# Kernel optimization log

Hardware: AMD Instinct MI355X
Metric: run time of the kernel (lower is better)

The kernel has to match this reference:

```python
import jax, jax.numpy as jnp
import numpy as np

# Production-scale 3D conv: B=4, C=64->64, 32^3 volume, 3x3x3 kernel, stride 1, pad 1.
B, CIN, COUT = 4, 64, 64
KSIZE = (3, 3, 3)
STRIDE = (1, 1, 1)
PAD = 1
SPATIAL = (32, 32, 32)


def setup_inputs() -> dict:
    key = jax.random.key(0)
    k1, k2, k3 = jax.random.split(key, 3)
    x = jax.random.normal(k1, (B, CIN) + SPATIAL, dtype=jnp.float32)
    weight = jax.random.normal(k2, (COUT, CIN) + KSIZE, dtype=jnp.float32)
    bias = jax.random.normal(k3, (COUT,), dtype=jnp.float32)
    return {"x": x, "weight": weight, "bias": bias}


def reference(x, weight, bias):
    # The original materializes all sliding-window patches via nested unfold and
    # contracts with einsum('bci...,oci->bo...'). That is exactly a standard
    # cross-correlation (torch-style conv). We express the same math as a direct
    # convolution, avoiding the O(kernel_volume) patch blowup.
    out = jax.lax.conv_general_dilated(
        x,
        weight,
        window_strides=STRIDE,
        padding=[(PAD, PAD)] * 3,
        dimension_numbers=("NCDHW", "OIDHW", "NCDHW"),
    )
    return out + bias.reshape(1, -1, 1, 1, 1)
```

## Files before the change

### kernel.cpp

```cpp
#include <hip/hip_runtime.h>
#include <hip/hip_bf16.h>

#define WS_W_OFF    0
#define WS_ZERO_OFF 221184
#define WS_XT_OFF   262144

typedef __attribute__((ext_vector_type(8))) short s16x8;
typedef __attribute__((ext_vector_type(4))) float f32x4;

#define GLOBAL_AS __attribute__((address_space(1)))
#define LDS_AS    __attribute__((address_space(3)))

__device__ __forceinline__ unsigned short f2bf(float f) {
  unsigned u = __builtin_bit_cast(unsigned, f);
  u = u + 0x7fffu + ((u >> 16) & 1u);
  return (unsigned short)(u >> 16);
}

__global__ void prep_kernel(const float* __restrict__ x,
                            const float* __restrict__ w,
                            unsigned short* __restrict__ wsw,
                            float* __restrict__ zeros,
                            unsigned short* __restrict__ xt) {
  int blk = blockIdx.x;
  int tid = threadIdx.x;
  if (blk < 432) {
    int t = blk * 256 + tid;
    int tap  = t % 27;
    int cin  = (t / 27) & 63;
    int cout = t / (27 * 64);
    int h   = cin >> 5;
    int q   = (cin >> 3) & 3;
    int j   = cin & 7;
    int nf  = cout >> 4;
    int lane = q * 16 + (cout & 15);
    int dst = (((tap * 2 + h) * 4 + nf) * 64 + lane) * 8 + j;
    wsw[dst] = f2bf(w[t]);
    if (t < 64) zeros[t] = 0.0f;
  } else {
    __shared__ __align__(16) unsigned char tile[256 * 144];
    int bi = blk - 432;
    int b  = bi >> 7;
    int s0 = (bi & 127) * 256;
    const float* xb = x + (size_t)b * 64 * 32768 + s0 + tid;
    #pragma unroll
    for (int c0 = 0; c0 < 64; c0 += 8) {
      s16x8 v;
      #pragma unroll
      for (int j = 0; j < 8; ++j)
        v[j] = (short)f2bf(xb[(size_t)(c0 + j) * 32768]);
      *(s16x8*)&tile[tid * 144 + c0 * 2] = v;
    }
    __syncthreads();
    #pragma unroll
    for (int it = 0; it < 8; ++it) {
      int row   = it * 32 + (tid >> 3);
      int col16 = tid & 7;
      s16x8 v = *(const s16x8*)&tile[row * 144 + col16 * 16];
      *(s16x8*)(xt + ((size_t)(b * 32768 + s0 + row) * 64 + col16 * 8)) = v;
    }
  }
}

__global__ __launch_bounds__(256, 2) void conv_kernel(const float* __restrict__ bias,
                                                      float* __restrict__ out,
                                                      const char* __restrict__ ws) {
  __shared__ __align__(16) unsigned char halo[52 * 1024];

  const int tid  = threadIdx.x;
  const int lane = tid & 63;
  const int w    = tid >> 6;
  const int logical = (blockIdx.x & 7) * 64 + (blockIdx.x >> 3);
  const int yt = logical & 7, zt = (logical >> 3) & 15, b = logical >> 7;
  const int z0 = zt * 2, y0 = yt * 4;
  const int zo  = w >> 1;
  const int yo2 = (w & 1) * 2;

  const int r15 = lane & 15;
  const int hi4 = lane >> 4;

  const int sl_sub   = lane >> 2;
  const int sl_chunk = lane & 3;

  auto stage_halo = [&](int h) {
    for (int g = w; g < 52; g += 4) {
      int pos = g * 16 + sl_sub;
      int hz = pos / 204; int rem = pos - hz * 204;
      int hy = rem / 34;  int hx = rem - hy * 34;
      int gz = z0 + hz - 1, gy = y0 + hy - 1, gx = hx - 1;
      bool inb = (pos < 816) & ((unsigned)gz < 32u) &
                 ((unsigned)gy < 32u) & ((unsigned)gx < 32u);
      int s = (gz * 32 + gy) * 32 + gx;
      int src = inb ? (WS_XT_OFF + (b * 32768 + s) * 128 + h * 64 + sl_chunk * 16)
                    : WS_ZERO_OFF;
      __builtin_amdgcn_global_load_lds(
          (const GLOBAL_AS void*)(ws + src),
          (LDS_AS void*)(&halo[g * 1024 + lane * 16]),
          16, 0, 0);
    }
  };

  const char* wsb_lane = ws + WS_W_OFF + lane * 16;

  f32x4 zero4 = {0.f, 0.f, 0.f, 0.f};
  f32x4 acc[4][4];
  #pragma unroll
  for (int mf = 0; mf < 4; ++mf)
    #pragma unroll
    for (int nf = 0; nf < 4; ++nf) acc[mf][nf] = zero4;

  s16x8 Bb[3][4];

  auto issueB = [&](int slot, int h, int tap) {
    const char* bt = wsb_lane + (tap * 2 + h) * 4096;
    asm volatile("global_load_dwordx4 %0, %1, off"             : "=v"(Bb[slot][0]) : "v"(bt));
    asm volatile("global_load_dwordx4 %0, %1, off offset:1024" : "=v"(Bb[slot][1]) : "v"(bt));
    asm volatile("global_load_dwordx4 %0, %1, off offset:2048" : "=v"(Bb[slot][2]) : "v"(bt));
    asm volatile("global_load_dwordx4 %0, %1, off offset:3072" : "=v"(Bb[slot][3]) : "v"(bt));
  };

  auto loadA = [&](s16x8* a, int tap) {
    int kd = tap / 9; int r9 = tap - kd * 9;
    int kh = r9 / 3;  int kw = r9 - kh * 3;
    int base = ((zo + kd) * 6 + (yo2 + kh)) * 34 + kw + r15;
    #pragma unroll
    for (int mf = 0; mf < 4; ++mf) {
      int pos = base + (mf >> 1) * 34 + (mf & 1) * 16;
      a[mf] = *(const s16x8*)&halo[pos * 64 + hi4 * 16];
    }
  };

  auto compute = [&](const s16x8* a, const s16x8* B) {
    #pragma unroll
    for (int mf = 0; mf < 4; ++mf)
      #pragma unroll
      for (int nf = 0; nf < 4; ++nf)
        acc[mf][nf] = __builtin_amdgcn_mfma_f32_16x16x32_bf16(
            a[mf], B[nf], acc[mf][nf], 0, 0, 0);
  };

  auto run27 = [&](int h) {
    #pragma unroll
    for (int tap = 0; tap < 27; ++tap) {
      if (tap < 25) issueB((tap + 2) % 3, h, tap + 2);
      if (tap < 25)        { asm volatile("s_waitcnt vmcnt(8)"); }
      else if (tap == 25)  { asm volatile("s_waitcnt vmcnt(4)"); }
      else                 { asm volatile("s_waitcnt vmcnt(0)"); }
      __builtin_amdgcn_sched_barrier(0x106);
      s16x8 Af[4];
      loadA(Af, tap);
      compute(Af, Bb[tap % 3]);
    }
  };

  stage_halo(0);
  issueB(0, 0, 0); issueB(1, 0, 1);
  __syncthreads();
  run27(0);

  issueB(0, 1, 0); issueB(1, 1, 1);
  __syncthreads();
  stage_halo(1);
  __syncthreads();
  run27(1);

  const int z = z0 + zo;
  #pragma unroll
  for (int nf = 0; nf < 4; ++nf) {
    int cout = nf * 16 + r15;
    float bv = bias[cout];
    #pragma unroll
    for (int mf = 0; mf < 4; ++mf) {
      int y  = y0 + yo2 + (mf >> 1);
      int x0 = (mf & 1) * 16 + 4 * hi4;
      float* orow = out + ((size_t)((b * 64 + cout) * 32 + z) * 32 + y) * 32;
      f32x4 v;
      #pragma unroll
      for (int r = 0; r < 4; ++r) v[r] = acc[mf][nf][r] + bv;
      *(f32x4*)&orow[x0] = v;
    }
  }
}

extern "C" void kernel_launch(void* const* d_in, const int* in_sizes, int n_in,
                              void* d_out, int out_size, void* d_ws, size_t ws_size,
                              hipStream_t stream) {
  const float* x    = (const float*)d_in[0];
  const float* wgt  = (const float*)d_in[1];
  const float* bias = (const float*)d_in[2];
  float* out = (float*)d_out;
  char* ws = (char*)d_ws;

  prep_kernel<<<944, 256, 0, stream>>>(x, wgt,
                                       (unsigned short*)(ws + WS_W_OFF),
                                       (float*)(ws + WS_ZERO_OFF),
                                       (unsigned short*)(ws + WS_XT_OFF));
  conv_kernel<<<512, 256, 0, stream>>>(bias, out, ws);
}
```

Before: 44.96 us.

## Stage weights through LDS with double-buffered register prefetch and barriers

Weight tiles are now copied cooperatively into a two-slot LDS buffer with global_load_lds, one 16-byte chunk per thread, so each block fetches a tap's weights once instead of every wave loading its own copy into registers. A/B fragments are prefetched one tap ahead into double-buffered registers, and MFMA issue is wrapped in setprio. This removes redundant global weight traffic per wave but adds several block-wide barriers per tap and more LDS reads. The rotation writing slot t&1 while slot t&1 is also read looks fragile, so the hazard ordering is questionable.

```diff
diff --git a/kernel.cpp b/kernel.cpp
--- a/kernel.cpp
+++ b/kernel.cpp
@@ -66,6 +66,7 @@
                                                       float* __restrict__ out,
                                                       const char* __restrict__ ws) {
   __shared__ __align__(16) unsigned char halo[52 * 1024];
+  __shared__ __align__(16) unsigned char blds[2][4096];
 
   const int tid  = threadIdx.x;
   const int lane = tid & 63;
@@ -100,7 +101,29 @@
     }
   };
 
-  const char* wsb_lane = ws + WS_W_OFF + lane * 16;
+  auto stage_B = [&](int h, int tap, int buf) {
+    __builtin_amdgcn_global_load_lds(
+        (const GLOBAL_AS void*)(ws + WS_W_OFF + (tap * 2 + h) * 4096 + tid * 16),
+        (LDS_AS void*)(&blds[buf][tid * 16]),
+        16, 0, 0);
+  };
+
+  auto loadBlds = [&](s16x8* dst, int buf) {
+    #pragma unroll
+    for (int nf = 0; nf < 4; ++nf)
+      dst[nf] = *(const s16x8*)&blds[buf][(nf * 64 + lane) * 16];
+  };
+
+  auto loadA = [&](s16x8* a, int tap) {
+    int kd = tap / 9; int r9 = tap - kd * 9;
+    int kh = r9 / 3;  int kw = r9 - kh * 3;
+    int base = ((zo + kd) * 6 + (yo2 + kh)) * 34 + kw + r15;
+    #pragma unroll
+    for (int mf = 0; mf < 4; ++mf) {
+      int pos = base + (mf >> 1) * 34 + (mf & 1) * 16;
+      a[mf] = *(const s16x8*)&halo[pos * 64 + hi4 * 16];
+    }
+  };
 
   f32x4 zero4 = {0.f, 0.f, 0.f, 0.f};
   f32x4 acc[4][4];
@@ -109,26 +132,7 @@
     #pragma unroll
     for (int nf = 0; nf < 4; ++nf) acc[mf][nf] = zero4;
 
-  s16x8 Bb[3][4];
-
-  auto issueB = [&](int slot, int h, int tap) {
-    const char* bt = wsb_lane + (tap * 2 + h) * 4096;
-    asm volatile("global_load_dwordx4 %0, %1, off"             : "=v"(Bb[slot][0]) : "v"(bt));
-    asm volatile("global_load_dwordx4 %0, %1, off offset:1024" : "=v"(Bb[slot][1]) : "v"(bt));
-    asm volatile("global_load_dwordx4 %0, %1, off offset:2048" : "=v"(Bb[slot][2]) : "v"(bt));
-    asm volatile("global_load_dwordx4 %0, %1, off offset:3072" : "=v"(Bb[slot][3]) : "v"(bt));
-  };
-
-  auto loadA = [&](s16x8* a, int tap) {
-    int kd = tap / 9; int r9 = tap - kd * 9;
-    int kh = r9 / 3;  int kw = r9 - kh * 3;
-    int base = ((zo + kd) * 6 + (yo2 + kh)) * 34 + kw + r15;
-    #pragma unroll
-    for (int mf = 0; mf < 4; ++mf) {
-      int pos = base + (mf >> 1) * 34 + (mf & 1) * 16;
-      a[mf] = *(const s16x8*)&halo[pos * 64 + hi4 * 16];
-    }
-  };
+  s16x8 Ar[2][4], Br[2][4];
 
   auto compute = [&](const s16x8* a, const s16x8* B) {
     #pragma unroll
@@ -140,27 +144,39 @@
   };
 
   auto run27 = [&](int h) {
-    #pragma unroll
-    for (int tap = 0; tap < 27; ++tap) {
-      if (tap < 25) issueB((tap + 2) % 3, h, tap + 2);
-      if (tap < 25)        { asm volatile("s_waitcnt vmcnt(8)"); }
-      else if (tap == 25)  { asm volatile("s_waitcnt vmcnt(4)"); }
-      else                 { asm volatile("s_waitcnt vmcnt(0)"); }
-      __builtin_amdgcn_sched_barrier(0x106);
-      s16x8 Af[4];
-      loadA(Af, tap);
-      compute(Af, Bb[tap % 3]);
+    loadBlds(Br[0], 0); loadA(Ar[0], 0);
+    asm volatile("s_waitcnt lgkmcnt(0)");
+    __builtin_amdgcn_s_barrier();
+    #pragma unroll
+    for (int t = 0; t < 27; ++t) {
+      const int cur = t & 1, nxt = cur ^ 1;
+      if (t + 2 <= 26) {
+        stage_B(h, t + 2, t & 1);
+        asm volatile("s_waitcnt vmcnt(1)");
+      } else if (t + 1 <= 26) {
+        asm volatile("s_waitcnt vmcnt(0)");
+      }
+      if (t + 1 <= 26) {
+        loadBlds(Br[nxt], (t + 1) & 1);
+        loadA(Ar[nxt], t + 1);
+      }
+      __builtin_amdgcn_s_barrier();
+      asm volatile("s_waitcnt lgkmcnt(0)");
+      __builtin_amdgcn_sched_barrier(0);
+      __builtin_amdgcn_s_setprio(1);
+      compute(Ar[cur], Br[cur]);
+      __builtin_amdgcn_s_setprio(0);
+      __builtin_amdgcn_s_barrier();
     }
   };
 
   stage_halo(0);
-  issueB(0, 0, 0); issueB(1, 0, 1);
+  stage_B(0, 0, 0); stage_B(0, 1, 1);
   __syncthreads();
   run27(0);
 
-  issueB(0, 1, 0); issueB(1, 1, 1);
-  __syncthreads();
   stage_halo(1);
+  stage_B(1, 0, 0); stage_B(1, 1, 1);
   __syncthreads();
   run27(1);
 
```

After: 52.86 us. +17.6%, slower.
